# Performance work log

Measured on AMD Instinct MI355X. Metric: run time of the kernel, lower is better.

Reference implementation:

```python
import jax, jax.numpy as jnp
import numpy as np

K = 16  # number of orientations; F = 1 + K*J filters
N = 512
F = 257  # 1 + K*J with J = 16

def setup_inputs() -> dict:
    key = jax.random.key(0)
    k1, k2, k3 = jax.random.split(key, 3)
    x_hat = jax.random.normal(k1, (N, N, 2), dtype=jnp.float32)
    psi_hat_real = jax.random.normal(k2, (F, N, N), dtype=jnp.float32)
    psi_hat_imag = jax.random.normal(k3, (F, N, N), dtype=jnp.float32)
    return {"x_hat": x_hat, "psi_hat_real": psi_hat_real, "psi_hat_imag": psi_hat_imag}

def reference(x_hat, psi_hat_real, psi_hat_imag):
    n = psi_hat_real.shape[1]
    # complex frequency-domain product  (broadcast single image against F filters)
    xc = x_hat[..., 0] + 1j * x_hat[..., 1]            # [n, n] complex
    psic = psi_hat_real + 1j * psi_hat_imag            # [F, n, n]
    conv = jnp.fft.ifft2(xc[None, :, :] * psic)        # [F, n, n] complex
    m = jnp.sqrt(conv.real ** 2 + conv.imag ** 2 + 1e-8)  # modulus [F, n, n]
    a = m[0]                                           # low-pass channel [n, n]
    p = m[1:].reshape(K, -1, n, n)                     # [K, J, n, n]
    J = p.shape[1]
    inv_nn = 1.0 / (n * n)
    s0 = jnp.mean(a ** 2)[None]                        # [1]
    # per-channel stats (spatial means)
    E2 = jnp.mean(p ** 2, axis=(2, 3))                 # [K, J]
    Ea = jnp.mean(p * a, axis=(2, 3))                  # [K, J]
    # pairwise covariances, one fused contraction each (replaces the KxJ python loop)
    C1 = jnp.einsum('kjnm,ljnm->klj', p, p) * inv_nn   # [K, K, J] cross-orientation
    C2 = jnp.einsum('kjnm,klnm->kjl', p, p) * inv_nn   # [K, J, J] cross-scale
    # assemble in the exact ordering of the original nested loop
    parts = [s0]
    for i in range(K):
        for j in range(J):
            parts.append(jnp.stack([E2[i, j], Ea[i, j]]))
            if i < K - 1:
                parts.append(C1[i, i + 1:, j])
            if j < J - 1:
                parts.append(C2[i, j, j + 1:])
    return jnp.concatenate(parts, axis=0)
```

## Files before the change

### kernel.cpp

```cpp
#include <hip/hip_runtime.h>
#include <hip/hip_fp16.h>
#include <stdint.h>
#include <stddef.h>

#define NL   512
#define NF   257
#define NNE  (NL*NL)
#define TWO_PI_OVER_N 0.012271846303085130f

__device__ __forceinline__ unsigned short f2bf(float x) {
  unsigned int u = __float_as_uint(x);
  u += 0x7fffu + ((u >> 16) & 1u);
  return (unsigned short)(u >> 16);
}

typedef __attribute__((ext_vector_type(8))) short bf16x8;
typedef __attribute__((ext_vector_type(4))) float f32x4;

__global__ __launch_bounds__(256) void pass1_rows(const float* __restrict__ x,
                                                  const float* __restrict__ pr,
                                                  const float* __restrict__ pi,
                                                  __half2* __restrict__ W,
                                                  int f0) {
  __shared__ float Xr[NL], Xi[NL];
  __shared__ float2 tw[256];
  const int t  = threadIdx.x;
  const int r  = blockIdx.x;
  const int fb = blockIdx.y;
  const int f  = f0 + fb;

  { float s, c; __sincosf((float)t * TWO_PI_OVER_N, &s, &c); tw[t] = make_float2(c, s); }

  const float2* xrow = (const float2*)(x + (size_t)r * (2 * NL));
  const size_t prow = ((size_t)f * NL + r) * NL;
  const int c0 = t, c1 = t + 256;
  {
    float2 xv = xrow[c0];
    float p0r = pr[prow + c0], p0i = pi[prow + c0];
    Xr[c0] = xv.x * p0r - xv.y * p0i;
    Xi[c0] = xv.x * p0i + xv.y * p0r;
    float2 xw = xrow[c1];
    float p1r = pr[prow + c1], p1i = pi[prow + c1];
    Xr[c1] = xw.x * p1r - xw.y * p1i;
    Xi[c1] = xw.x * p1i + xw.y * p1r;
  }
  __syncthreads();

  for (int lh = 8; lh >= 0; --lh) {
    const int h  = 1 << lh;
    const int k  = t & (h - 1);
    const int i0 = ((t >> lh) << (lh + 1)) + k;
    const int i1 = i0 + h;
    float ar = Xr[i0], ai = Xi[i0], br = Xr[i1], bi = Xi[i1];
    float2 w = tw[k << (8 - lh)];
    Xr[i0] = ar + br;  Xi[i0] = ai + bi;
    float dr = ar - br, di = ai - bi;
    Xr[i1] = w.x * dr - w.y * di;
    Xi[i1] = w.x * di + w.y * dr;
    __syncthreads();
  }

  __half2* Wrow = W + ((size_t)fb * NL + r) * NL;
  Wrow[c0] = __floats2half2_rn(Xr[c0], Xi[c0]);
  Wrow[c1] = __floats2half2_rn(Xr[c1], Xi[c1]);
}

#define P2S 513
__global__ __launch_bounds__(512) void pass2_cols(const __half2* __restrict__ W,
                                                  unsigned short* __restrict__ m,
                                                  int f0) {
  __shared__ __half2 XX[16 * P2S];
  __shared__ __half2 twA[256], twB[256];
  const int t    = threadIdx.x;
  const int tile = blockIdx.x;
  const int fb   = blockIdx.y;
  const int f    = f0 + fb;
  const int c0   = tile * 16;

  if (t < 256) {
    float s, c; __sincosf((float)t * TWO_PI_OVER_N, &s, &c);
    twA[t] = __floats2half2_rn(c, c);
    twB[t] = __floats2half2_rn(-s, s);
  }

  const uint4* Wp4 = (const uint4*)(W + (size_t)fb * NNE);
#pragma unroll
  for (int it = 0; it < 4; ++it) {
    int sl = it * 512 + t;
    int r = sl >> 2, g = sl & 3;
    uint4 v = Wp4[r * 128 + (c0 >> 2) + g];
    int cl = g * 4;
    XX[(cl + 0) * P2S + r] = *(__half2*)&v.x;
    XX[(cl + 1) * P2S + r] = *(__half2*)&v.y;
    XX[(cl + 2) * P2S + r] = *(__half2*)&v.z;
    XX[(cl + 3) * P2S + r] = *(__half2*)&v.w;
  }
  __syncthreads();

  const int col = t >> 5;
  const int b0  = t & 31;
  const int cb  = col * P2S;
  const __half2 mI = __floats2half2_rn(-1.f, 1.f);

  for (int lh = 8; lh >= 2; lh -= 2) {
    const int hh = 1 << (lh - 1);
#pragma unroll
    for (int q = 0; q < 4; ++q) {
      int p  = b0 + q * 32;
      int k  = p & (hh - 1);
      int B  = (p >> (lh - 1)) << (lh + 1);
      int i0 = cb + B + k, i1 = i0 + hh, i2 = i0 + 2 * hh, i3 = i0 + 3 * hh;
      __half2 e0 = XX[i0], e1 = XX[i1], e2 = XX[i2], e3 = XX[i3];
      int kA = k << (8 - lh), kB = k << (9 - lh);
      __half2 aA = twA[kA], bA = twB[kA];
      __half2 aB = twA[kB], bB = twB[kB];
      __half2 f0v = __hadd2(e0, e2);
      __half2 f1v = __hadd2(e1, e3);
      __half2 d02 = __hsub2(e0, e2);
      __half2 d13 = __hsub2(e1, e3);
      __half2 f2v = __hfma2(d02, aA, __hmul2(__lowhigh2highlow(d02), bA));
      __half2 t3  = __hfma2(d13, aA, __hmul2(__lowhigh2highlow(d13), bA));
      __half2 f3v = __hmul2(__lowhigh2highlow(t3), mI);
      XX[i0] = __hadd2(f0v, f1v);
      __half2 d01 = __hsub2(f0v, f1v);
      XX[i1] = __hfma2(d01, aB, __hmul2(__lowhigh2highlow(d01), bB));
      XX[i2] = __hadd2(f2v, f3v);
      __half2 d23 = __hsub2(f2v, f3v);
      XX[i3] = __hfma2(d23, aB, __hmul2(__lowhigh2highlow(d23), bB));
    }
    __syncthreads();
  }

  const float inv = 1.0f / (float)NNE;
  unsigned int* mp = (unsigned int*)(m + (size_t)f * NNE + (size_t)(c0 + col) * NL);
#pragma unroll
  for (int u = 0; u < 8; ++u) {
    int p = b0 + u * 32;
    __half2 a = XX[cb + 2 * p], b = XX[cb + 2 * p + 1];
    float2 af = __half22float2(a), bf = __half22float2(b);
    float r0 = (af.x + bf.x) * inv, s0 = (af.y + bf.y) * inv;
    float r1 = (af.x - bf.x) * inv, s1 = (af.y - bf.y) * inv;
    float m0 = sqrtf(r0 * r0 + s0 * s0 + 1e-8f);
    float m1 = sqrtf(r1 * r1 + s1 * s1 + 1e-8f);
    mp[p] = (unsigned int)f2bf(m0) | ((unsigned int)f2bf(m1) << 16);
  }
}

__global__ __launch_bounds__(256) void gram_kernel(const unsigned short* __restrict__ m,
                                                   float* __restrict__ G) {
  const int chunk = blockIdx.x;
  const int g     = blockIdx.y;
  const int wave  = threadIdx.x >> 6;
  const int lane  = threadIdx.x & 63;
  const int mrow  = lane & 15;
  const int quad  = lane >> 4;
  const int pidx  = (g < 16) ? (1 + mrow * 16 + g) : (1 + (g - 16) * 16 + mrow);
  const unsigned short* plane = m + (size_t)pidx * NNE;
  const int base0 = chunk * 8192 + wave * 2048 + quad * 8;

  f32x4 acc = {0.f, 0.f, 0.f, 0.f};
#pragma unroll 4
  for (int it = 0; it < 64; ++it) {
    bf16x8 frag = *(const bf16x8*)(plane + base0 + it * 32);
    acc = __builtin_amdgcn_mfma_f32_16x16x32_bf16(frag, frag, acc, 0, 0, 0);
  }
  const int colo = lane & 15;
  const int row0 = quad * 4;
#pragma unroll
  for (int rr = 0; rr < 4; ++rr)
    atomicAdd(&G[g * 256 + (row0 + rr) * 16 + colo], acc[rr]);
}

__global__ __launch_bounds__(256) void ea_kernel(const unsigned short* __restrict__ m,
                                                 float* __restrict__ EA) {
  const int f = blockIdx.x, chunk = blockIdx.y, t = threadIdx.x;
  const unsigned short* p = m + (size_t)f * NNE + chunk * 16384;
  const unsigned short* a = m + chunk * 16384;
  float acc = 0.f;
  for (int it = 0; it < 8; ++it) {
    int off = (it * 256 + t) * 8;
    uint4 up = *(const uint4*)(p + off);
    uint4 ua = *(const uint4*)(a + off);
    const unsigned int pw[4] = {up.x, up.y, up.z, up.w};
    const unsigned int aw[4] = {ua.x, ua.y, ua.z, ua.w};
#pragma unroll
    for (int q = 0; q < 4; ++q) {
      acc += __uint_as_float(pw[q] << 16) * __uint_as_float(aw[q] << 16);
      acc += __uint_as_float(pw[q] & 0xffff0000u) * __uint_as_float(aw[q] & 0xffff0000u);
    }
  }
  __shared__ float red[256];
  red[t] = acc; __syncthreads();
  for (int w = 128; w > 0; w >>= 1) { if (t < w) red[t] += red[t + w]; __syncthreads(); }
  if (t == 0) atomicAdd(&EA[f], red[0]);
}

__global__ void zero_acc(float* g) {
  int i = blockIdx.x * 256 + threadIdx.x;
  if (i < 8449) g[i] = 0.f;
}

__global__ __launch_bounds__(256) void assemble_kernel(const float* __restrict__ G,
                                                       const float* __restrict__ EA,
                                                       float* __restrict__ out) {
  const float inv = 1.0f / (float)NNE;
  const int t = threadIdx.x;
  const int i = t >> 4, j = t & 15;
  int base = 1;
  for (int c = 0; c < t; ++c) {
    int ci = c >> 4, cj = c & 15;
    base += 2 + (15 - ci) + (15 - cj);
  }
  if (t == 0) out[0] = EA[0] * inv;
  float* o = out + base;
  int n = 0;
  o[n++] = G[j * 256 + i * 16 + i] * inv;
  o[n++] = EA[1 + i * 16 + j] * inv;
  for (int l = i + 1; l < 16; ++l)
    o[n++] = G[j * 256 + i * 16 + l] * inv;
  for (int l = j + 1; l < 16; ++l)
    o[n++] = G[(16 + i) * 256 + j * 16 + l] * inv;
}

extern "C" void kernel_launch(void* const* d_in, const int* in_sizes, int n_in,
                              void* d_out, int out_size, void* d_ws, size_t ws_size,
                              hipStream_t stream) {
  const float* x  = (const float*)d_in[0];
  const float* pr = (const float*)d_in[1];
  const float* pi = (const float*)d_in[2];
  float* out = (float*)d_out;
  char* ws = (char*)d_ws;

  unsigned short* m = (unsigned short*)ws;
  const size_t g_off = (size_t)NF * NNE * 2;
  float* G  = (float*)(ws + g_off);
  float* EA = (float*)(ws + g_off + 32768);
  const size_t w_off = g_off + 33808;
  __half2* W = (__half2*)(ws + w_off);

  size_t avail = ws_size > w_off ? ws_size - w_off : 0;
  int BF = (int)(avail / ((size_t)NNE * 4));
  if (BF < 1)  BF = 1;
  if (BF > NF) BF = NF;

  zero_acc<<<34, 256, 0, stream>>>(G);

  for (int f0 = 0; f0 < NF; f0 += BF) {
    int bf = NF - f0 < BF ? NF - f0 : BF;
    pass1_rows<<<dim3(512, bf), 256, 0, stream>>>(x, pr, pi, W, f0);
    pass2_cols<<<dim3(32, bf), 512, 0, stream>>>(W, m, f0);
  }

  gram_kernel<<<dim3(32, 32), 256, 0, stream>>>(m, G);
  ea_kernel<<<dim3(NF, 16), 256, 0, stream>>>(m, EA);
  assemble_kernel<<<1, 256, 0, stream>>>(G, EA, out);
}
```

Baseline: 873.1 us.

## Switch row FFT to radix-4 with two rows per block and swizzled LDS

```diff
diff --git a/kernel.cpp b/kernel.cpp
--- a/kernel.cpp
+++ b/kernel.cpp
@@ -16,53 +16,101 @@
 
 typedef __attribute__((ext_vector_type(8))) short bf16x8;
 typedef __attribute__((ext_vector_type(4))) float f32x4;
+
+__device__ __forceinline__ int swz(int i) {
+  return i ^ (((i >> 2) & 24) | ((i >> 4) & 6));
+}
 
 __global__ __launch_bounds__(256) void pass1_rows(const float* __restrict__ x,
                                                   const float* __restrict__ pr,
                                                   const float* __restrict__ pi,
                                                   __half2* __restrict__ W,
                                                   int f0) {
-  __shared__ float Xr[NL], Xi[NL];
-  __shared__ float2 tw[256];
-  const int t  = threadIdx.x;
-  const int r  = blockIdx.x;
-  const int fb = blockIdx.y;
-  const int f  = f0 + fb;
-
-  { float s, c; __sincosf((float)t * TWO_PI_OVER_N, &s, &c); tw[t] = make_float2(c, s); }
-
-  const float2* xrow = (const float2*)(x + (size_t)r * (2 * NL));
+  __shared__ float Xr[2 * NL], Xi[2 * NL];
+  __shared__ float4 twp[170];
+  const int t    = threadIdx.x;
+  const int half = t >> 7;
+  const int p    = t & 127;
+  const int r    = blockIdx.x * 2 + half;
+  const int fb   = blockIdx.y;
+  const int f    = f0 + fb;
+  const int base = half * NL;
+
+  if (t < 170) {
+    int s_  = (t < 128) ? 0 : (t < 160) ? 1 : (t < 168) ? 2 : 3;
+    int off = (s_ == 0) ? 0 : (s_ == 1) ? 128 : (s_ == 2) ? 160 : 168;
+    int k   = t - off;
+    float ang = (float)(k << (2 * s_)) * TWO_PI_OVER_N;
+    float sA, cA, sB, cB;
+    __sincosf(ang, &sA, &cA);
+    __sincosf(2.f * ang, &sB, &cB);
+    twp[t] = make_float4(cA, sA, cB, sB);
+  }
+
   const size_t prow = ((size_t)f * NL + r) * NL;
-  const int c0 = t, c1 = t + 256;
+  const float4* pr4 = (const float4*)(pr + prow);
+  const float4* pi4 = (const float4*)(pi + prow);
+  const float4* xr4 = (const float4*)(x + (size_t)r * (2 * NL));
   {
-    float2 xv = xrow[c0];
-    float p0r = pr[prow + c0], p0i = pi[prow + c0];
-    Xr[c0] = xv.x * p0r - xv.y * p0i;
-    Xi[c0] = xv.x * p0i + xv.y * p0r;
-    float2 xw = xrow[c1];
-    float p1r = pr[prow + c1], p1i = pi[prow + c1];
-    Xr[c1] = xw.x * p1r - xw.y * p1i;
-    Xi[c1] = xw.x * p1i + xw.y * p1r;
+    float4 a  = pr4[p];
+    float4 b  = pi4[p];
+    float4 x0 = xr4[2 * p];
+    float4 x1 = xr4[2 * p + 1];
+    float v0r = x0.x * a.x - x0.y * b.x, v0i = x0.x * b.x + x0.y * a.x;
+    float v1r = x0.z * a.y - x0.w * b.y, v1i = x0.z * b.y + x0.w * a.y;
+    float v2r = x1.x * a.z - x1.y * b.z, v2i = x1.x * b.z + x1.y * a.z;
+    float v3r = x1.z * a.w - x1.w * b.w, v3i = x1.z * b.w + x1.w * a.w;
+    int s0i = base + swz(4 * p);
+    int s1i = base + swz(4 * p + 2);
+    *(float2*)&Xr[s0i] = make_float2(v0r, v1r);
+    *(float2*)&Xr[s1i] = make_float2(v2r, v3r);
+    *(float2*)&Xi[s0i] = make_float2(v0i, v1i);
+    *(float2*)&Xi[s1i] = make_float2(v2i, v3i);
   }
   __syncthreads();
 
-  for (int lh = 8; lh >= 0; --lh) {
-    const int h  = 1 << lh;
-    const int k  = t & (h - 1);
-    const int i0 = ((t >> lh) << (lh + 1)) + k;
-    const int i1 = i0 + h;
-    float ar = Xr[i0], ai = Xi[i0], br = Xr[i1], bi = Xi[i1];
-    float2 w = tw[k << (8 - lh)];
-    Xr[i0] = ar + br;  Xi[i0] = ai + bi;
-    float dr = ar - br, di = ai - bi;
-    Xr[i1] = w.x * dr - w.y * di;
-    Xi[i1] = w.x * di + w.y * dr;
+#pragma unroll
+  for (int s_ = 0; s_ < 4; ++s_) {
+    const int lh  = 8 - 2 * s_;
+    const int hh  = 1 << (lh - 1);
+    const int off = (s_ == 0) ? 0 : (s_ == 1) ? 128 : (s_ == 2) ? 160 : 168;
+    const int k   = p & (hh - 1);
+    const int j0  = ((p >> (lh - 1)) << (lh + 1)) + k;
+    const int i0  = base + swz(j0);
+    const int i1  = base + swz(j0 + hh);
+    const int i2  = base + swz(j0 + 2 * hh);
+    const int i3  = base + swz(j0 + 3 * hh);
+    float4 w = twp[off + k];
+    float e0r = Xr[i0], e0i = Xi[i0], e2r = Xr[i2], e2i = Xi[i2];
+    float e1r = Xr[i1], e1i = Xi[i1], e3r = Xr[i3], e3i = Xi[i3];
+    float f0r = e0r + e2r, f0i = e0i + e2i;
+    float f1r = e1r + e3r, f1i = e1i + e3i;
+    float d2r = e0r - e2r, d2i = e0i - e2i;
+    float d3r = e1r - e3r, d3i = e1i - e3i;
+    float g2r = d2r * w.x - d2i * w.y, g2i = d2i * w.x + d2r * w.y;
+    float t3r = d3r * w.x - d3i * w.y, t3i = d3i * w.x + d3r * w.y;
+    float g3r = -t3i, g3i = t3r;
+    Xr[i0] = f0r + f1r;  Xi[i0] = f0i + f1i;
+    float d0r = f0r - f1r, d0i = f0i - f1i;
+    Xr[i1] = d0r * w.z - d0i * w.w;  Xi[i1] = d0i * w.z + d0r * w.w;
+    Xr[i2] = g2r + g3r;  Xi[i2] = g2i + g3i;
+    float d1r = g2r - g3r, d1i = g2i - g3i;
+    Xr[i3] = d1r * w.z - d1i * w.w;  Xi[i3] = d1i * w.z + d1r * w.w;
     __syncthreads();
   }
 
   __half2* Wrow = W + ((size_t)fb * NL + r) * NL;
-  Wrow[c0] = __floats2half2_rn(Xr[c0], Xi[c0]);
-  Wrow[c1] = __floats2half2_rn(Xr[c1], Xi[c1]);
+#pragma unroll
+  for (int u = 0; u < 2; ++u) {
+    int q  = p + u * 128;
+    int a0 = base + swz(2 * q);
+    float2 rr = *(const float2*)&Xr[a0];
+    float2 ri = *(const float2*)&Xi[a0];
+    union { float2 fv; __half2 h[2]; } pk;
+    pk.h[0] = __floats2half2_rn(rr.x + rr.y, ri.x + ri.y);
+    pk.h[1] = __floats2half2_rn(rr.x - rr.y, ri.x - ri.y);
+    ((float2*)Wrow)[q] = pk.fv;
+  }
 }
 
 #define P2S 513
@@ -70,17 +118,26 @@
                                                   unsigned short* __restrict__ m,
                                                   int f0) {
   __shared__ __half2 XX[16 * P2S];
-  __shared__ __half2 twA[256], twB[256];
+  __shared__ uint2 twAB[170];
+  __shared__ uint2 twCD[170];
   const int t    = threadIdx.x;
   const int tile = blockIdx.x;
   const int fb   = blockIdx.y;
   const int f    = f0 + fb;
   const int c0   = tile * 16;
 
-  if (t < 256) {
-    float s, c; __sincosf((float)t * TWO_PI_OVER_N, &s, &c);
-    twA[t] = __floats2half2_rn(c, c);
-    twB[t] = __floats2half2_rn(-s, s);
+  if (t < 170) {
+    int s_  = (t < 128) ? 0 : (t < 160) ? 1 : (t < 168) ? 2 : 3;
+    int off = (s_ == 0) ? 0 : (s_ == 1) ? 128 : (s_ == 2) ? 160 : 168;
+    int k   = t - off;
+    float ang = (float)(k << (2 * s_)) * TWO_PI_OVER_N;
+    float sn, cs;
+    __sincosf(ang, &sn, &cs);
+    __half2 a = __floats2half2_rn(cs, cs), b = __floats2half2_rn(-sn, sn);
+    twAB[t] = make_uint2(*(unsigned int*)&a, *(unsigned int*)&b);
+    __sincosf(2.f * ang, &sn, &cs);
+    a = __floats2half2_rn(cs, cs); b = __floats2half2_rn(-sn, sn);
+    twCD[t] = make_uint2(*(unsigned int*)&a, *(unsigned int*)&b);
   }
 
   const uint4* Wp4 = (const uint4*)(W + (size_t)fb * NNE);
@@ -102,8 +159,11 @@
   const int cb  = col * P2S;
   const __half2 mI = __floats2half2_rn(-1.f, 1.f);
 
-  for (int lh = 8; lh >= 2; lh -= 2) {
-    const int hh = 1 << (lh - 1);
+#pragma unroll
+  for (int s_ = 0; s_ < 4; ++s_) {
+    const int lh  = 8 - 2 * s_;
+    const int hh  = 1 << (lh - 1);
+    const int off = (s_ == 0) ? 0 : (s_ == 1) ? 128 : (s_ == 2) ? 160 : 168;
 #pragma unroll
     for (int q = 0; q < 4; ++q) {
       int p  = b0 + q * 32;
@@ -111,9 +171,10 @@
       int B  = (p >> (lh - 1)) << (lh + 1);
       int i0 = cb + B + k, i1 = i0 + hh, i2 = i0 + 2 * hh, i3 = i0 + 3 * hh;
       __half2 e0 = XX[i0], e1 = XX[i1], e2 = XX[i2], e3 = XX[i3];
-      int kA = k << (8 - lh), kB = k << (9 - lh);
-      __half2 aA = twA[kA], bA = twB[kA];
-      __half2 aB = twA[kB], bB = twB[kB];
+      uint2 vA = twAB[off + k];
+      uint2 vB = twCD[off + k];
+      __half2 aA = *(__half2*)&vA.x, bA = *(__half2*)&vA.y;
+      __half2 aB = *(__half2*)&vB.x, bB = *(__half2*)&vB.y;
       __half2 f0v = __hadd2(e0, e2);
       __half2 f1v = __hadd2(e1, e3);
       __half2 d02 = __hsub2(e0, e2);
@@ -247,7 +308,7 @@
 
   for (int f0 = 0; f0 < NF; f0 += BF) {
     int bf = NF - f0 < BF ? NF - f0 : BF;
-    pass1_rows<<<dim3(512, bf), 256, 0, stream>>>(x, pr, pi, W, f0);
+    pass1_rows<<<dim3(256, bf), 256, 0, stream>>>(x, pr, pi, W, f0);
     pass2_cols<<<dim3(32, bf), 512, 0, stream>>>(W, m, f0);
   }
 
```

After: 747.3 us. -14.4%, faster.
